# Kernel optimization log

Hardware: AMD Instinct MI355X
Metric: run time of the kernel (lower is better)

Reference implementation:

```python
import jax, jax.numpy as jnp
import numpy as np

B, D, T, C = 128, 128, 2048, 64


def setup_inputs() -> dict:
    key = jax.random.key(0)
    k1, k2, k3 = jax.random.split(key, 3)
    feature = jax.random.normal(k1, (B, D, T), dtype=jnp.float32)
    label = jax.random.randint(k2, (B, T), 0, C, dtype=jnp.int64)
    centers = jax.random.normal(k3, (C, D), dtype=jnp.float32)
    return {"feature": feature, "label": label, "centers": centers}


def reference(feature, label, centers):
    # feature: [B, D, T] -> flatten to [N, D] with N = B*T (transpose(2,1).reshape)
    num_classes, feat_dim = centers.shape
    feat = jnp.transpose(feature, (0, 2, 1)).reshape(-1, feat_dim)  # [N, D]
    lab = label.reshape(-1)                                          # [N]

    centers_batch = centers[lab]                                     # gather [N, D]
    center_loss = jnp.mean((feat - centers_batch) ** 2)              # MSELoss (mean)

    diff = centers_batch - feat                                      # [N, D]
    # scatter-sum of per-row diffs into their class slot (replaces python loop)
    difference = jax.ops.segment_sum(diff, lab, num_segments=num_classes)  # [C, D]
    appear_times = jnp.bincount(lab, length=num_classes)             # [C]
    difference = difference / jnp.clip(appear_times, 1, None).astype(difference.dtype)[:, None]
    return (center_loss, difference)
```

## Files before the change

### kernel.cpp

```cpp
#include <hip/hip_runtime.h>


#define NT 2048
#define NC 64
#define TQ 512
#define RB 520

#define OFF_S     0
#define OFF_CNT   8192
#define OFF_SSP   8256
#define OFF_CROSS 9280
#define OFF_CC    9536
#define OFF_P     9792
#define WS_NEED_BYTES ((size_t)(OFF_P + 1024 * 4096) * 4)

template <bool PARTIAL>
__global__ __launch_bounds__(256) void k_main(const float* __restrict__ feat,
                                              const int*  __restrict__ label,
                                              float* __restrict__ ws) {
    __shared__ float __attribute__((aligned(16))) rowbuf[4][2][RB];
    __shared__ unsigned short __attribute__((aligned(16))) sorted[1024];
    __shared__ float S_lds[NC][65];
    __shared__ float red[256];
    __shared__ int cnt[NC], pstart[NC], cursor[NC];
    __shared__ unsigned char gclass[192];

    const int tid = threadIdx.x, bid = blockIdx.x;
    const int b = bid >> 3, dh = (bid >> 2) & 1, th = bid & 3;
    const int w = tid >> 6, lane = tid & 63;

    for (int j = tid; j < 1024; j += 256) sorted[j] = (unsigned short)2048;
    if (tid < NC) { cnt[tid] = 0; cursor[tid] = 0; }
    if (tid < 192) gclass[tid] = 0;
    for (int j = tid; j < NC * 65; j += 256) ((float*)S_lds)[j] = 0.0f;
    if (tid < 64) rowbuf[tid >> 4][(tid >> 3) & 1][512 + (tid & 7)] = 0.0f;
    __syncthreads();

    const int* lp = label + b * NT + th * TQ + tid * 2;
    const int2 L = *(const int2*)lp;
    atomicAdd(&cnt[L.x], 1); atomicAdd(&cnt[L.y], 1);
    __syncthreads();

    if (tid == 0) {
        int pt = 0;
        for (int c = 0; c < NC; ++c) {
            int pl = (cnt[c] + 3) & ~3;
            pstart[c] = pt; pt += pl;
        }
    }
    __syncthreads();

    if (tid < NC) {
        int g0 = pstart[tid] >> 2;
        int g1 = g0 + (((cnt[tid] + 3) & ~3) >> 2);
        for (int g = g0; g < g1; ++g) gclass[g] = (unsigned char)tid;
    }
    {
        int p = pstart[L.x] + atomicAdd(&cursor[L.x], 1);
        sorted[p] = (unsigned short)((tid * 2 + 0) * 4);
        p = pstart[L.y] + atomicAdd(&cursor[L.y], 1);
        sorted[p] = (unsigned short)((tid * 2 + 1) * 4);
    }
    __syncthreads();

    int offs[3][4]; int cls[3];
    #pragma unroll
    for (int g3 = 0; g3 < 3; ++g3) {
        const int g = lane + 64 * g3;
        const uint2 pk = *(const uint2*)&sorted[g * 4];
        offs[g3][0] = pk.x & 0xFFFF; offs[g3][1] = pk.x >> 16;
        offs[g3][2] = pk.y & 0xFFFF; offs[g3][3] = pk.y >> 16;
        cls[g3] = gclass[g];
    }

    const float* fbase = feat + ((size_t)b * 128 + dh * 64) * NT + th * TQ;
    float ssA = 0.0f, ssB = 0.0f;

    float4 a0, b0, a1, b1;
    {
        const float* rp0 = fbase + (size_t)w * NT;
        const float* rp1 = fbase + (size_t)(w + 4) * NT;
        a0 = *(const float4*)(rp0 + lane * 4);
        b0 = *(const float4*)(rp0 + 256 + lane * 4);
        a1 = *(const float4*)(rp1 + lane * 4);
        b1 = *(const float4*)(rp1 + 256 + lane * 4);
    }

    #pragma unroll
    for (int i = 0; i < 16; ++i) {
        const int sl = i & 1;
        float* dst = &rowbuf[w][sl][0];
        if (sl == 0) {
            *(float4*)(dst + lane * 4)       = a0;
            *(float4*)(dst + 256 + lane * 4) = b0;
            if (i + 2 < 16) {
                const float* rp = fbase + (size_t)(w + 4 * (i + 2)) * NT;
                a0 = *(const float4*)(rp + lane * 4);
                b0 = *(const float4*)(rp + 256 + lane * 4);
            }
        } else {
            *(float4*)(dst + lane * 4)       = a1;
            *(float4*)(dst + 256 + lane * 4) = b1;
            if (i + 2 < 16) {
                const float* rp = fbase + (size_t)(w + 4 * (i + 2)) * NT;
                a1 = *(const float4*)(rp + lane * 4);
                b1 = *(const float4*)(rp + 256 + lane * 4);
            }
        }
        const char* rb = (const char*)dst;
        const int dslot = w + 4 * i;
        #pragma unroll
        for (int g3 = 0; g3 < 3; ++g3) {
            float v0 = *(const float*)(rb + offs[g3][0]);
            float v1 = *(const float*)(rb + offs[g3][1]);
            float v2 = *(const float*)(rb + offs[g3][2]);
            float v3 = *(const float*)(rb + offs[g3][3]);
            ssA += v0 * v0 + v1 * v1;
            ssB += v2 * v2 + v3 * v3;
            atomicAdd(&S_lds[cls[g3]][dslot], (v0 + v1) + (v2 + v3));
        }
    }

    if (dh == 0 && tid < NC) atomicAdd((int*)(ws + OFF_CNT) + tid, cnt[tid]);

    __syncthreads();
    if (PARTIAL) {
        const int c = tid >> 2, j0 = (tid & 3) * 16;
        float* gP = ws + OFF_P + (size_t)bid * 4096 + c * 64 + j0;
        float4 v0, v1, v2, v3;
        v0.x = S_lds[c][j0 +  0]; v0.y = S_lds[c][j0 +  1];
        v0.z = S_lds[c][j0 +  2]; v0.w = S_lds[c][j0 +  3];
        v1.x = S_lds[c][j0 +  4]; v1.y = S_lds[c][j0 +  5];
        v1.z = S_lds[c][j0 +  6]; v1.w = S_lds[c][j0 +  7];
        v2.x = S_lds[c][j0 +  8]; v2.y = S_lds[c][j0 +  9];
        v2.z = S_lds[c][j0 + 10]; v2.w = S_lds[c][j0 + 11];
        v3.x = S_lds[c][j0 + 12]; v3.y = S_lds[c][j0 + 13];
        v3.z = S_lds[c][j0 + 14]; v3.w = S_lds[c][j0 + 15];
        *(float4*)gP        = v0;
        *(float4*)(gP + 4)  = v1;
        *(float4*)(gP + 8)  = v2;
        *(float4*)(gP + 12) = v3;
    } else {
        const int c = tid >> 2, j0 = (tid & 3) * 16;
        float* gS = ws + OFF_S + (size_t)c * 128 + dh * 64 + j0;
        #pragma unroll
        for (int j = 0; j < 16; ++j) atomicAdd(&gS[j], S_lds[c][j0 + j]);
    }

    red[tid] = ssA + ssB;
    __syncthreads();
    for (int s = 128; s > 0; s >>= 1) {
        if (tid < s) red[tid] += red[tid + s];
        __syncthreads();
    }
    if (tid == 0) ws[OFF_SSP + bid] = red[0];
}

__global__ __launch_bounds__(256) void k_red_p(float* __restrict__ ws,
                                               const float* __restrict__ centers,
                                               float* __restrict__ out) {
    const int tid = threadIdx.x, bid = blockIdx.x;
    const int j = tid & 31, s = tid >> 5;
    const int e = bid * 32 + j;
    const int c = e >> 7, d = e & 127, dhh = d >> 6, dl = d & 63;

    const float* base = ws + OFF_P + ((size_t)dhh * 4) * 4096 + c * 64 + dl;
    float sum = 0.0f;
    for (int b = s * 16; b < s * 16 + 16; ++b) {
        const float* pb = base + (size_t)b * 8 * 4096;
        sum += (pb[0] + pb[4096]) + (pb[2 * 4096] + pb[3 * 4096]);
    }

    __shared__ float red[256];
    red[tid] = sum;
    __syncthreads();
    if (tid < 128) red[tid] += red[tid + 128];
    __syncthreads();
    if (tid < 64)  red[tid] += red[tid + 64];
    __syncthreads();

    if (tid < 32) {
        const float tot = red[tid] + red[tid + 32];
        const float cn  = (float)((const int*)(ws + OFF_CNT))[c];
        const float ctr = centers[e];
        const float den = cn > 1.0f ? cn : 1.0f;
        out[1 + e] = (cn * ctr - tot) / den;

        float r1 = tot * ctr;
        float r2 = cn * ctr * ctr;
        for (int o = 16; o > 0; o >>= 1) {
            r1 += __shfl_down(r1, o, 32);
            r2 += __shfl_down(r2, o, 32);
        }
        if (tid == 0) { ws[OFF_CROSS + bid] = r1; ws[OFF_CC + bid] = r2; }
    }
}

__global__ __launch_bounds__(256) void k_red_a(float* __restrict__ ws,
                                               const float* __restrict__ centers,
                                               float* __restrict__ out) {
    const int tid = threadIdx.x, bid = blockIdx.x;
    const int e = bid * 256 + tid, c = e >> 7;
    const float sum = ws[OFF_S + e];
    const float cn  = (float)((const int*)(ws + OFF_CNT))[c];
    const float ctr = centers[e];
    const float den = cn > 1.0f ? cn : 1.0f;
    out[1 + e] = (cn * ctr - sum) / den;

    __shared__ float r1[256], r2[256];
    r1[tid] = sum * ctr;
    r2[tid] = cn * ctr * ctr;
    __syncthreads();
    for (int k = 128; k > 0; k >>= 1) {
        if (tid < k) { r1[tid] += r1[tid + k]; r2[tid] += r2[tid + k]; }
        __syncthreads();
    }
    if (tid == 0) { ws[OFF_CROSS + bid] = r1[0]; ws[OFF_CC + bid] = r2[0]; }
}

__global__ __launch_bounds__(256) void k_epi(const float* __restrict__ ws,
                                             float* __restrict__ out,
                                             int ncross) {
    const int tid = threadIdx.x;
    __shared__ float r[256];
    float s = ws[OFF_SSP + tid] + ws[OFF_SSP + tid + 256]
            + ws[OFF_SSP + tid + 512] + ws[OFF_SSP + tid + 768];
    if (tid < ncross) s += ws[OFF_CC + tid] - 2.0f * ws[OFF_CROSS + tid];
    r[tid] = s;
    __syncthreads();
    for (int k = 128; k > 0; k >>= 1) {
        if (tid < k) r[tid] += r[tid + k];
        __syncthreads();
    }
    if (tid == 0) out[0] = r[0] * (1.0f / 33554432.0f);
}

extern "C" void kernel_launch(void* const* d_in, const int* in_sizes, int n_in,
                              void* d_out, int out_size, void* d_ws, size_t ws_size,
                              hipStream_t stream) {
    const float* feat    = (const float*)d_in[0];
    const int*   label   = (const int*)d_in[1];
    const float* centers = (const float*)d_in[2];
    float* out = (float*)d_out;
    float* ws  = (float*)d_ws;

    hipMemsetAsync(ws, 0, 8256 * sizeof(float), stream);

    if (ws_size >= WS_NEED_BYTES) {
        hipLaunchKernelGGL(k_main<true>,  dim3(1024), dim3(256), 0, stream, feat, label, ws);
        hipLaunchKernelGGL(k_red_p, dim3(256), dim3(256), 0, stream, ws, centers, out);
        hipLaunchKernelGGL(k_epi,   dim3(1),   dim3(256), 0, stream, ws, out, 256);
    } else {
        hipLaunchKernelGGL(k_main<false>, dim3(1024), dim3(256), 0, stream, feat, label, ws);
        hipLaunchKernelGGL(k_red_a, dim3(32),  dim3(256), 0, stream, ws, centers, out);
        hipLaunchKernelGGL(k_epi,   dim3(1),   dim3(256), 0, stream, ws, out, 32);
    }
}
```

Before: 248.4 us.

## Replace label-sorted LDS staging with direct per-element LDS atomics

Removes the per-block counting sort of labels (prefix sums, sorted offsets, class groups) and the rowbuf LDS staging of feature rows. Each lane now reads its features straight from registers and does one LDS atomicAdd per element into the class row of S_lds, and the global prefetch becomes a triple-buffered register pipeline. This cuts several barriers and the setup work, but raises the number of LDS atomics from about 3 to 8 per row per lane, and those atomics may contend when labels collide.

```diff
diff --git a/kernel.cpp b/kernel.cpp
--- a/kernel.cpp
+++ b/kernel.cpp
@@ -4,7 +4,6 @@
 #define NT 2048
 #define NC 64
 #define TQ 512
-#define RB 520
 
 #define OFF_S     0
 #define OFF_CNT   8192
@@ -18,107 +17,81 @@
 __global__ __launch_bounds__(256) void k_main(const float* __restrict__ feat,
                                               const int*  __restrict__ label,
                                               float* __restrict__ ws) {
-    __shared__ float __attribute__((aligned(16))) rowbuf[4][2][RB];
-    __shared__ unsigned short __attribute__((aligned(16))) sorted[1024];
     __shared__ float S_lds[NC][65];
     __shared__ float red[256];
-    __shared__ int cnt[NC], pstart[NC], cursor[NC];
-    __shared__ unsigned char gclass[192];
+    __shared__ int cnt[NC];
 
     const int tid = threadIdx.x, bid = blockIdx.x;
     const int b = bid >> 3, dh = (bid >> 2) & 1, th = bid & 3;
     const int w = tid >> 6, lane = tid & 63;
 
-    for (int j = tid; j < 1024; j += 256) sorted[j] = (unsigned short)2048;
-    if (tid < NC) { cnt[tid] = 0; cursor[tid] = 0; }
-    if (tid < 192) gclass[tid] = 0;
     for (int j = tid; j < NC * 65; j += 256) ((float*)S_lds)[j] = 0.0f;
-    if (tid < 64) rowbuf[tid >> 4][(tid >> 3) & 1][512 + (tid & 7)] = 0.0f;
-    __syncthreads();
-
-    const int* lp = label + b * NT + th * TQ + tid * 2;
-    const int2 L = *(const int2*)lp;
-    atomicAdd(&cnt[L.x], 1); atomicAdd(&cnt[L.y], 1);
-    __syncthreads();
-
-    if (tid == 0) {
-        int pt = 0;
-        for (int c = 0; c < NC; ++c) {
-            int pl = (cnt[c] + 3) & ~3;
-            pstart[c] = pt; pt += pl;
-        }
-    }
-    __syncthreads();
-
-    if (tid < NC) {
-        int g0 = pstart[tid] >> 2;
-        int g1 = g0 + (((cnt[tid] + 3) & ~3) >> 2);
-        for (int g = g0; g < g1; ++g) gclass[g] = (unsigned char)tid;
-    }
+    if (tid < NC) cnt[tid] = 0;
+    __syncthreads();
+
+    const int* lbase = label + b * NT + th * TQ;
     {
-        int p = pstart[L.x] + atomicAdd(&cursor[L.x], 1);
-        sorted[p] = (unsigned short)((tid * 2 + 0) * 4);
-        p = pstart[L.y] + atomicAdd(&cursor[L.y], 1);
-        sorted[p] = (unsigned short)((tid * 2 + 1) * 4);
-    }
-    __syncthreads();
-
-    int offs[3][4]; int cls[3];
-    #pragma unroll
-    for (int g3 = 0; g3 < 3; ++g3) {
-        const int g = lane + 64 * g3;
-        const uint2 pk = *(const uint2*)&sorted[g * 4];
-        offs[g3][0] = pk.x & 0xFFFF; offs[g3][1] = pk.x >> 16;
-        offs[g3][2] = pk.y & 0xFFFF; offs[g3][3] = pk.y >> 16;
-        cls[g3] = gclass[g];
-    }
+        const int2 L = *(const int2*)(lbase + tid * 2);
+        atomicAdd(&cnt[L.x], 1); atomicAdd(&cnt[L.y], 1);
+    }
+
+    const int4 LA = *(const int4*)(lbase + 4 * lane);
+    const int4 LB = *(const int4*)(lbase + 256 + 4 * lane);
+    char* const Sb = (char*)&S_lds[0][0];
+    const int o0 = LA.x * 260, o1 = LA.y * 260, o2 = LA.z * 260, o3 = LA.w * 260;
+    const int o4 = LB.x * 260, o5 = LB.y * 260, o6 = LB.z * 260, o7 = LB.w * 260;
 
     const float* fbase = feat + ((size_t)b * 128 + dh * 64) * NT + th * TQ;
     float ssA = 0.0f, ssB = 0.0f;
 
-    float4 a0, b0, a1, b1;
+    float4 A0, B0, A1, B1, A2, B2;
     {
-        const float* rp0 = fbase + (size_t)w * NT;
-        const float* rp1 = fbase + (size_t)(w + 4) * NT;
-        a0 = *(const float4*)(rp0 + lane * 4);
-        b0 = *(const float4*)(rp0 + 256 + lane * 4);
-        a1 = *(const float4*)(rp1 + lane * 4);
-        b1 = *(const float4*)(rp1 + 256 + lane * 4);
+        const float* r0 = fbase + (size_t)(w     ) * NT;
+        const float* r1 = fbase + (size_t)(w +  4) * NT;
+        const float* r2 = fbase + (size_t)(w +  8) * NT;
+        A0 = *(const float4*)(r0 + 4 * lane); B0 = *(const float4*)(r0 + 256 + 4 * lane);
+        A1 = *(const float4*)(r1 + 4 * lane); B1 = *(const float4*)(r1 + 256 + 4 * lane);
+        A2 = *(const float4*)(r2 + 4 * lane); B2 = *(const float4*)(r2 + 256 + 4 * lane);
     }
 
     #pragma unroll
     for (int i = 0; i < 16; ++i) {
-        const int sl = i & 1;
-        float* dst = &rowbuf[w][sl][0];
+        float4 a, bb;
+        const int sl = i % 3;
         if (sl == 0) {
-            *(float4*)(dst + lane * 4)       = a0;
-            *(float4*)(dst + 256 + lane * 4) = b0;
-            if (i + 2 < 16) {
-                const float* rp = fbase + (size_t)(w + 4 * (i + 2)) * NT;
-                a0 = *(const float4*)(rp + lane * 4);
-                b0 = *(const float4*)(rp + 256 + lane * 4);
+            a = A0; bb = B0;
+            if (i + 3 < 16) {
+                const float* rp = fbase + (size_t)(w + 4 * (i + 3)) * NT;
+                A0 = *(const float4*)(rp + 4 * lane);
+                B0 = *(const float4*)(rp + 256 + 4 * lane);
+            }
+        } else if (sl == 1) {
+            a = A1; bb = B1;
+            if (i + 3 < 16) {
+                const float* rp = fbase + (size_t)(w + 4 * (i + 3)) * NT;
+                A1 = *(const float4*)(rp + 4 * lane);
+                B1 = *(const float4*)(rp + 256 + 4 * lane);
             }
         } else {
-            *(float4*)(dst + lane * 4)       = a1;
-            *(float4*)(dst + 256 + lane * 4) = b1;
-            if (i + 2 < 16) {
-                const float* rp = fbase + (size_t)(w + 4 * (i + 2)) * NT;
-                a1 = *(const float4*)(rp + lane * 4);
-                b1 = *(const float4*)(rp + 256 + lane * 4);
+            a = A2; bb = B2;
+            if (i + 3 < 16) {
+                const float* rp = fbase + (size_t)(w + 4 * (i + 3)) * NT;
+                A2 = *(const float4*)(rp + 4 * lane);
+                B2 = *(const float4*)(rp + 256 + 4 * lane);
             }
         }
-        const char* rb = (const char*)dst;
-        const int dslot = w + 4 * i;
-        #pragma unroll
-        for (int g3 = 0; g3 < 3; ++g3) {
-            float v0 = *(const float*)(rb + offs[g3][0]);
-            float v1 = *(const float*)(rb + offs[g3][1]);
-            float v2 = *(const float*)(rb + offs[g3][2]);
-            float v3 = *(const float*)(rb + offs[g3][3]);
-            ssA += v0 * v0 + v1 * v1;
-            ssB += v2 * v2 + v3 * v3;
-            atomicAdd(&S_lds[cls[g3]][dslot], (v0 + v1) + (v2 + v3));
-        }
+
+        const int db = (w + 4 * i) << 2;
+        atomicAdd((float*)(Sb + o0 + db), a.x);
+        atomicAdd((float*)(Sb + o1 + db), a.y);
+        atomicAdd((float*)(Sb + o2 + db), a.z);
+        atomicAdd((float*)(Sb + o3 + db), a.w);
+        atomicAdd((float*)(Sb + o4 + db), bb.x);
+        atomicAdd((float*)(Sb + o5 + db), bb.y);
+        atomicAdd((float*)(Sb + o6 + db), bb.z);
+        atomicAdd((float*)(Sb + o7 + db), bb.w);
+        ssA += a.x * a.x + a.y * a.y + a.z * a.z + a.w * a.w;
+        ssB += bb.x * bb.x + bb.y * bb.y + bb.z * bb.z + bb.w * bb.w;
     }
 
     if (dh == 0 && tid < NC) atomicAdd((int*)(ws + OFF_CNT) + tid, cnt[tid]);
```

Result: slower. 327.6 us (+31.9%).

## Assign one class per lane and accumulate class sums in registers

Applied to the files above, without the earlier changes.

The per-tile work is remapped so each lane owns one class and walks that class's sorted token offsets, accumulating sums and squared sums in registers. Each wave now processes 16 consecutive feature rows instead of interleaved rows. This removes the LDS float atomics into S_lds, along with the padded group/class tables and their initialisation. The cost is lane divergence from uneven class counts, which forces predicated work up to the wave maximum, plus a slow fallback loop for classes with more than 24 tokens.

```diff
diff --git a/kernel.cpp b/kernel.cpp
--- a/kernel.cpp
+++ b/kernel.cpp
@@ -5,6 +5,7 @@
 #define NC 64
 #define TQ 512
 #define RB 520
+#define UNR 24
 
 #define OFF_S     0
 #define OFF_CNT   8192
@@ -19,42 +20,29 @@
                                               const int*  __restrict__ label,
                                               float* __restrict__ ws) {
     __shared__ float __attribute__((aligned(16))) rowbuf[4][2][RB];
-    __shared__ unsigned short __attribute__((aligned(16))) sorted[1024];
+    __shared__ unsigned short __attribute__((aligned(16))) sorted[512];
     __shared__ float S_lds[NC][65];
     __shared__ float red[256];
     __shared__ int cnt[NC], pstart[NC], cursor[NC];
-    __shared__ unsigned char gclass[192];
 
     const int tid = threadIdx.x, bid = blockIdx.x;
     const int b = bid >> 3, dh = (bid >> 2) & 1, th = bid & 3;
     const int w = tid >> 6, lane = tid & 63;
 
-    for (int j = tid; j < 1024; j += 256) sorted[j] = (unsigned short)2048;
     if (tid < NC) { cnt[tid] = 0; cursor[tid] = 0; }
-    if (tid < 192) gclass[tid] = 0;
-    for (int j = tid; j < NC * 65; j += 256) ((float*)S_lds)[j] = 0.0f;
-    if (tid < 64) rowbuf[tid >> 4][(tid >> 3) & 1][512 + (tid & 7)] = 0.0f;
-    __syncthreads();
-
-    const int* lp = label + b * NT + th * TQ + tid * 2;
-    const int2 L = *(const int2*)lp;
+    __syncthreads();
+
+    const int* lbase = label + b * NT + th * TQ;
+    const int2 L = *(const int2*)(lbase + tid * 2);
     atomicAdd(&cnt[L.x], 1); atomicAdd(&cnt[L.y], 1);
     __syncthreads();
 
     if (tid == 0) {
         int pt = 0;
-        for (int c = 0; c < NC; ++c) {
-            int pl = (cnt[c] + 3) & ~3;
-            pstart[c] = pt; pt += pl;
-        }
-    }
-    __syncthreads();
-
-    if (tid < NC) {
-        int g0 = pstart[tid] >> 2;
-        int g1 = g0 + (((cnt[tid] + 3) & ~3) >> 2);
-        for (int g = g0; g < g1; ++g) gclass[g] = (unsigned char)tid;
-    }
+        for (int c = 0; c < NC; ++c) { pstart[c] = pt; pt += cnt[c]; }
+    }
+    __syncthreads();
+
     {
         int p = pstart[L.x] + atomicAdd(&cursor[L.x], 1);
         sorted[p] = (unsigned short)((tid * 2 + 0) * 4);
@@ -63,63 +51,69 @@
     }
     __syncthreads();
 
-    int offs[3][4]; int cls[3];
-    #pragma unroll
-    for (int g3 = 0; g3 < 3; ++g3) {
-        const int g = lane + 64 * g3;
-        const uint2 pk = *(const uint2*)&sorted[g * 4];
-        offs[g3][0] = pk.x & 0xFFFF; offs[g3][1] = pk.x >> 16;
-        offs[g3][2] = pk.y & 0xFFFF; offs[g3][3] = pk.y >> 16;
-        cls[g3] = gclass[g];
-    }
+    const int cl = cnt[lane], ps = pstart[lane];
+    int off[UNR];
+    #pragma unroll
+    for (int j = 0; j < UNR; ++j) off[j] = (j < cl) ? (int)sorted[ps + j] : 0;
+
+    int wm = cl;
+    #pragma unroll
+    for (int o = 32; o >= 1; o >>= 1) { int t = __shfl_xor(wm, o); wm = wm > t ? wm : t; }
 
     const float* fbase = feat + ((size_t)b * 128 + dh * 64) * NT + th * TQ;
-    float ssA = 0.0f, ssB = 0.0f;
-
-    float4 a0, b0, a1, b1;
+    float acc[16];
+    #pragma unroll
+    for (int j = 0; j < 16; ++j) acc[j] = 0.0f;
+    float ss = 0.0f;
+
+    float4 Ae, Be, Ao, Bo;
     {
-        const float* rp0 = fbase + (size_t)w * NT;
-        const float* rp1 = fbase + (size_t)(w + 4) * NT;
-        a0 = *(const float4*)(rp0 + lane * 4);
-        b0 = *(const float4*)(rp0 + 256 + lane * 4);
-        a1 = *(const float4*)(rp1 + lane * 4);
-        b1 = *(const float4*)(rp1 + 256 + lane * 4);
+        const float* r0 = fbase + (size_t)(16 * w) * NT;
+        const float* r1 = fbase + (size_t)(16 * w + 1) * NT;
+        Ae = *(const float4*)(r0 + 4 * lane); Be = *(const float4*)(r0 + 256 + 4 * lane);
+        Ao = *(const float4*)(r1 + 4 * lane); Bo = *(const float4*)(r1 + 256 + 4 * lane);
+    }
+    {
+        float* d0 = &rowbuf[w][0][0];
+        *(float4*)(d0 + 4 * lane) = Ae; *(float4*)(d0 + 256 + 4 * lane) = Be;
     }
 
     #pragma unroll
     for (int i = 0; i < 16; ++i) {
-        const int sl = i & 1;
-        float* dst = &rowbuf[w][sl][0];
-        if (sl == 0) {
-            *(float4*)(dst + lane * 4)       = a0;
-            *(float4*)(dst + 256 + lane * 4) = b0;
+        const char* rb = (const char*)&rowbuf[w][i & 1][0];
+        #pragma unroll
+        for (int qb = 0; qb < UNR / 4; ++qb) {
+            if (qb * 4 < wm) {
+                #pragma unroll
+                for (int k = 0; k < 4; ++k) {
+                    const int j = qb * 4 + k;
+                    if (j < cl) {
+                        const float v = *(const float*)(rb + off[j]);
+                        acc[i] += v; ss += v * v;
+                    }
+                }
+            }
+        }
+        if (cl > UNR) {
+            for (int j = UNR; j < cl; ++j) {
+                const float v = *(const float*)(rb + (int)sorted[ps + j]);
+                acc[i] += v; ss += v * v;
+            }
+        }
+        if (i < 15) {
+            float* dst = &rowbuf[w][(i + 1) & 1][0];
+            if ((i + 1) & 1) { *(float4*)(dst + 4 * lane) = Ao; *(float4*)(dst + 256 + 4 * lane) = Bo; }
+            else             { *(float4*)(dst + 4 * lane) = Ae; *(float4*)(dst + 256 + 4 * lane) = Be; }
             if (i + 2 < 16) {
-                const float* rp = fbase + (size_t)(w + 4 * (i + 2)) * NT;
-                a0 = *(const float4*)(rp + lane * 4);
-                b0 = *(const float4*)(rp + 256 + lane * 4);
+                const float* rp = fbase + (size_t)(16 * w + i + 2) * NT;
+                if (i & 1) { Ao = *(const float4*)(rp + 4 * lane); Bo = *(const float4*)(rp + 256 + 4 * lane); }
+                else       { Ae = *(const float4*)(rp + 4 * lane); Be = *(const float4*)(rp + 256 + 4 * lane); }
             }
-        } else {
-            *(float4*)(dst + lane * 4)       = a1;
-            *(float4*)(dst + 256 + lane * 4) = b1;
-            if (i + 2 < 16) {
-                const float* rp = fbase + (size_t)(w + 4 * (i + 2)) * NT;
-                a1 = *(const float4*)(rp + lane * 4);
-                b1 = *(const float4*)(rp + 256 + lane * 4);
-            }
-        }
-        const char* rb = (const char*)dst;
-        const int dslot = w + 4 * i;
-        #pragma unroll
-        for (int g3 = 0; g3 < 3; ++g3) {
-            float v0 = *(const float*)(rb + offs[g3][0]);
-            float v1 = *(const float*)(rb + offs[g3][1]);
-            float v2 = *(const float*)(rb + offs[g3][2]);
-            float v3 = *(const float*)(rb + offs[g3][3]);
-            ssA += v0 * v0 + v1 * v1;
-            ssB += v2 * v2 + v3 * v3;
-            atomicAdd(&S_lds[cls[g3]][dslot], (v0 + v1) + (v2 + v3));
-        }
-    }
+        }
+    }
+
+    #pragma unroll
+    for (int j = 0; j < 16; ++j) S_lds[lane][16 * w + j] = acc[j];
 
     if (dh == 0 && tid < NC) atomicAdd((int*)(ws + OFF_CNT) + tid, cnt[tid]);
 
@@ -147,7 +141,7 @@
         for (int j = 0; j < 16; ++j) atomicAdd(&gS[j], S_lds[c][j0 + j]);
     }
 
-    red[tid] = ssA + ssB;
+    red[tid] = ss;
     __syncthreads();
     for (int s = 128; s > 0; s >>= 1) {
         if (tid < s) red[tid] += red[tid + s];
```

Result: faster. 212.8 us (-14.3%).
